# Kernel optimization log

Hardware: AMD Instinct MI355X
Metric: run time of the kernel (lower is better)

## Reference

```python
import jax, jax.numpy as jnp
import numpy as np

B, HW, ENC, E, D, A, V, L = 64, 14, 2048, 512, 512, 512, 32000, 32
LN_EPS = 1e-5


def setup_inputs() -> dict:
    key = jax.random.key(0)
    ks = jax.random.split(key, 16)
    s = 0.02
    n = lambda k, sh: jax.random.normal(k, sh, jnp.float32)
    encoder_out = n(ks[0], (B, HW, HW, ENC))
    encoded_captions = jax.random.randint(ks[1], (B, L), 0, V)
    caption_lengths = jax.random.randint(ks[2], (B, 1), 2, L + 1)
    caption_lengths = caption_lengths.at[0, 0].set(L)  # ensure max length present
    return dict(
        encoder_out=encoder_out,
        encoded_captions=encoded_captions,
        caption_lengths=caption_lengths,
        emb=n(ks[3], (V, E)) * s,
        W_enc_att=n(ks[4], (A, ENC)) * s, b_enc_att=jnp.zeros((A,)),
        W_dec_att=n(ks[5], (A, D)) * s, b_dec_att=jnp.zeros((A,)),
        W_full_att=n(ks[6], (1, A)) * s, b_full_att=jnp.zeros((1,)),
        W_ih=n(ks[7], (4 * D, E + ENC)) * s, b_ih=jnp.zeros((4 * D,)),
        W_hh=n(ks[8], (4 * D, D)) * s, b_hh=jnp.zeros((4 * D,)),
        g_h=jnp.ones((D,)), be_h=jnp.zeros((D,)),
        g_c=jnp.ones((D,)), be_c=jnp.zeros((D,)),
        W_init_h=n(ks[9], (D, ENC)) * s, b_init_h=jnp.zeros((D,)),
        W_init_c=n(ks[10], (D, ENC)) * s, b_init_c=jnp.zeros((D,)),
        W_beta=n(ks[11], (ENC, D)) * s, b_beta=jnp.zeros((ENC,)),
        W_fc=n(ks[12], (V, D)) * s, b_fc=jnp.zeros((V,)),
    )


def _layer_norm(x, g, b):
    m = x.mean(-1, keepdims=True)
    v = ((x - m) ** 2).mean(-1, keepdims=True)
    return (x - m) / jnp.sqrt(v + LN_EPS) * g + b


def reference(encoder_out, encoded_captions, caption_lengths, emb,
              W_enc_att, b_enc_att, W_dec_att, b_dec_att, W_full_att, b_full_att,
              W_ih, b_ih, W_hh, b_hh, g_h, be_h, g_c, be_c,
              W_init_h, b_init_h, W_init_c, b_init_c, W_beta, b_beta, W_fc, b_fc):
    bsz = encoder_out.shape[0]
    enc_out = encoder_out.reshape(bsz, -1, encoder_out.shape[-1])  # [B,P,ENC]
    lengths = caption_lengths[:, 0]
    order = jnp.argsort(-lengths)  # stable descending sort (matches torch sort)
    lengths = lengths[order]
    enc_out = enc_out[order]
    caps = encoded_captions[order]
    embeds = emb[caps]  # [B,L,E]
    decode_lengths = lengths - 1
    T = caps.shape[1] - 1  # static max(decode_lengths)

    mean_enc = enc_out.mean(axis=1)
    h = _layer_norm(mean_enc @ W_init_h.T + b_init_h, g_h, be_h)
    c = _layer_norm(mean_enc @ W_init_c.T + b_init_c, g_c, be_c)

    att1 = enc_out @ W_enc_att.T + b_enc_att  # [B,P,A] precomputed once
    prev_seq = jnp.swapaxes(embeds[:, :T], 0, 1)  # [T,B,E] teacher-forced inputs
    masks = jnp.arange(T)[:, None] < decode_lengths[None, :]  # [T,B] active rows

    def step(carry, xs):
        h, c = carry
        prev, mask = xs
        # attention
        att2 = h @ W_dec_att.T + b_dec_att  # [B,A]
        e = jax.nn.relu(att1 + att2[:, None, :]) @ W_full_att[0] + b_full_att[0]  # [B,P]
        alpha = jax.nn.softmax(e, axis=1)
        awe = jnp.einsum('bpe,bp->be', enc_out, alpha)  # [B,ENC]
        gate = jax.nn.sigmoid(h @ W_beta.T + b_beta)
        awe = gate * awe
        # LSTM cell
        x = jnp.concatenate([prev, awe], axis=1)  # [B,E+ENC]
        gates = x @ W_ih.T + b_ih + h @ W_hh.T + b_hh
        i, f, g, o = jnp.split(gates, 4, axis=1)
        c_new = jax.nn.sigmoid(f) * c + jax.nn.sigmoid(i) * jnp.tanh(g)
        h_new = jax.nn.sigmoid(o) * jnp.tanh(c_new)
        h_new = _layer_norm(h_new, g_h, be_h)
        c_new = _layer_norm(c_new, g_c, be_c)
        preds = h_new @ W_fc.T + b_fc  # [B,V]; dropout is identity in eval
        m = mask[:, None]
        h = jnp.where(m, h_new, h)  # freeze finished rows (== torch batch shrink)
        c = jnp.where(m, c_new, c)
        return (h, c), (jnp.where(m, preds, 0.0), jnp.where(m, alpha, 0.0))

    (_, _), (preds_t, alphas_t) = jax.lax.scan(step, (h, c), (prev_seq, masks))
    predictions = jnp.swapaxes(preds_t, 0, 1)  # [B,T,V]
    alphas = jnp.swapaxes(alphas_t, 0, 1)      # [B,T,P]
    return predictions, caps, decode_lengths, alphas, order
```

## Files before the change

kernel.cpp:

```cpp
#include <hip/hip_runtime.h>
#include <cfloat>
#include <math.h>

#define B_ 64
#define P_ 196
#define ENC_ 2048
#define D_ 512
#define V_ 32000
#define L_ 32
#define T_ 31

#define OUT_PREDS 0L
#define OUT_CAPS  63488000L
#define OUT_DECL  63490048L
#define OUT_ALPH  63490112L
#define OUT_ORDER 63878976L

typedef __bf16 bf16;
typedef __bf16 bf16x8 __attribute__((ext_vector_type(8)));
typedef __bf16 bf16x4 __attribute__((ext_vector_type(4)));
typedef float  f32x4  __attribute__((ext_vector_type(4)));

static __device__ __forceinline__ float sigmoidf_(float x) { return 1.f / (1.f + __expf(-x)); }

__global__ void k_order(const int* __restrict__ cap_len, const int* __restrict__ caps,
                        int* __restrict__ order_i, int* __restrict__ declen_i,
                        int* __restrict__ caps_i, float* __restrict__ out)
{
    __shared__ int len_s[B_];
    int tid = threadIdx.x;
    len_s[tid] = cap_len[tid];
    __syncthreads();
    int li = len_s[tid];
    int pos = 0;
    for (int j = 0; j < B_; ++j) {
        int lj = len_s[j];
        pos += (lj > li) || (lj == li && j < tid);
    }
    order_i[pos]  = tid;
    declen_i[pos] = li - 1;
    out[OUT_ORDER + pos] = (float)tid;
    out[OUT_DECL  + pos] = (float)(li - 1);
    for (int l = 0; l < L_; ++l) {
        int tok = caps[tid * L_ + l];
        caps_i[pos * L_ + l] = tok;
        out[OUT_CAPS + pos * L_ + l] = (float)tok;
    }
}

__global__ __launch_bounds__(256) void k_cvt(const float* __restrict__ in, bf16* __restrict__ ob, long n)
{
    long i = ((long)blockIdx.x * 256 + threadIdx.x) * 8;
    if (i >= n) return;
    float4 a = *(const float4*)(in + i);
    float4 b = *(const float4*)(in + i + 4);
    bf16x8 v;
    v[0]=(bf16)a.x; v[1]=(bf16)a.y; v[2]=(bf16)a.z; v[3]=(bf16)a.w;
    v[4]=(bf16)b.x; v[5]=(bf16)b.y; v[6]=(bf16)b.z; v[7]=(bf16)b.w;
    *(bf16x8*)(ob + i) = v;
}

__global__ __launch_bounds__(256) void k_cvt_enc(const float* __restrict__ enc,
                                                 const int* __restrict__ order_i,
                                                 bf16* __restrict__ enc_s)
{
    long i = ((long)blockIdx.x * 256 + threadIdx.x) * 8;
    int b = (int)(i / ((long)P_ * ENC_));
    long rem = i - (long)b * P_ * ENC_;
    const float* src = enc + (long)order_i[b] * P_ * ENC_ + rem;
    float4 a = *(const float4*)(src);
    float4 c = *(const float4*)(src + 4);
    bf16x8 v;
    v[0]=(bf16)a.x; v[1]=(bf16)a.y; v[2]=(bf16)a.z; v[3]=(bf16)a.w;
    v[4]=(bf16)c.x; v[5]=(bf16)c.y; v[6]=(bf16)c.z; v[7]=(bf16)c.w;
    *(bf16x8*)(enc_s + i) = v;
}

__global__ __launch_bounds__(256) void k_meanb(const bf16* __restrict__ enc_s, bf16* __restrict__ mean_b)
{
    int b = blockIdx.x, col = blockIdx.y * 256 + threadIdx.x;
    float s = 0.f;
    const bf16* eb = enc_s + (long)b * P_ * ENC_ + col;
    for (int p = 0; p < P_; ++p) s += (float)eb[(long)p * ENC_];
    mean_b[(long)b * ENC_ + col] = (bf16)(s * (1.f / (float)P_));
}

template<int FUSE, int EPI, int SWZ>
__global__ void __launch_bounds__(256)
k_mgemm(const bf16* __restrict__ A, long lda,
        const bf16* __restrict__ B1, const bf16* __restrict__ B2,
        const float* __restrict__ bias,
        float* __restrict__ Cf, bf16* __restrict__ Cb,
        int N, int K, int kspl, int Nsp, int Ksp,
        const int* __restrict__ declen_i)
{
    const int tid = threadIdx.x;
    const int lane = tid & 63, w = tid >> 6;
    int mt, nt, z;
    if (SWZ == 0)      { mt = blockIdx.x; nt = blockIdx.y; z = blockIdx.z; }
    else if (SWZ == 1) { int o = blockIdx.x; int wg = (o & 7) * 98 + (o >> 3);
                         mt = wg >> 2; nt = wg & 3; z = 0; }
    else               { int o = blockIdx.x; int xcd = o & 7;
                         int base = xcd < 6 ? xcd * 969 : 5814 + (xcd - 6) * 968;
                         int wg = base + (o >> 3);
                         nt = wg / 31; mt = wg - 31 * nt; z = 0; }
    const int krange = K / kspl;
    const int k0 = z * krange, k1 = k0 + krange;
    const int r16 = lane & 15, kq = lane >> 4;
    const int koff = kq * 8;

    const bf16* Ap = A + (long)(mt * 64 + r16) * lda + koff;
    const int ncol0 = nt * 128 + w * 32;

    const bf16* Bp[2];
    const bf16* B2p[2];
#pragma unroll
    for (int ni = 0; ni < 2; ++ni) {
        int n = ncol0 + ni * 16 + r16;
        if (FUSE == 1)
            Bp[ni] = (n < Nsp) ? B1 + (long)n * K + koff
                               : B2 + (long)(n - Nsp) * K + koff;
        else if (FUSE == 2) {
            Bp[ni]  = B1 + (long)n * Ksp + koff;
            B2p[ni] = B2 + (long)n * (K - Ksp) + koff - Ksp;
        } else
            Bp[ni] = B1 + (long)n * K + koff;
    }

    auto loadA = [&](int kk, bf16x8* dst) {
#pragma unroll
        for (int mi = 0; mi < 4; ++mi)
            dst[mi] = *(const bf16x8*)(Ap + (long)mi * 16 * lda + kk);
    };
    auto loadB = [&](int kk, bf16x8* dst) {
#pragma unroll
        for (int ni = 0; ni < 2; ++ni) {
            if (FUSE == 2 && kk >= Ksp) dst[ni] = *(const bf16x8*)(B2p[ni] + kk);
            else                        dst[ni] = *(const bf16x8*)(Bp[ni] + kk);
        }
    };

    f32x4 acc[4][2] = {};
    bf16x8 af[4], bfr[2];
    loadA(k0, af); loadB(k0, bfr);
    for (int kk = k0 + 32; kk < k1; kk += 32) {
        bf16x8 af2[4], bf2[2];
        loadA(kk, af2); loadB(kk, bf2);
#pragma unroll
        for (int mi = 0; mi < 4; ++mi)
#pragma unroll
            for (int ni = 0; ni < 2; ++ni)
                acc[mi][ni] = __builtin_amdgcn_mfma_f32_16x16x32_bf16(af[mi], bfr[ni], acc[mi][ni], 0, 0, 0);
#pragma unroll
        for (int mi = 0; mi < 4; ++mi) af[mi] = af2[mi];
#pragma unroll
        for (int ni = 0; ni < 2; ++ni) bfr[ni] = bf2[ni];
    }
#pragma unroll
    for (int mi = 0; mi < 4; ++mi)
#pragma unroll
        for (int ni = 0; ni < 2; ++ni)
            acc[mi][ni] = __builtin_amdgcn_mfma_f32_16x16x32_bf16(af[mi], bfr[ni], acc[mi][ni], 0, 0, 0);

#pragma unroll
    for (int mi = 0; mi < 4; ++mi) {
#pragma unroll
        for (int ni = 0; ni < 2; ++ni) {
            int col = ncol0 + ni * 16 + r16;
#pragma unroll
            for (int r = 0; r < 4; ++r) {
                int row = mt * 64 + mi * 16 + kq * 4 + r;
                float v = acc[mi][ni][r];
                if (EPI == 0) {
                    Cf[(long)z * 64 * N + (long)row * N + col] = v;
                } else if (EPI == 1) {
                    Cb[(long)row * N + col] = (bf16)(v + bias[col]);
                } else {
                    int tt = row >> 6, b = row & 63;
                    bool msk = tt < declen_i[b];
                    Cf[OUT_PREDS + ((long)b * T_ + tt) * V_ + col] = msk ? (v + bias[col]) : 0.f;
                }
            }
        }
    }
}

static __device__ __forceinline__ void ln_stats(float x, float* r1, float* r2,
                                                float& m, float& var)
{
    int tid = threadIdx.x;
    r1[tid] = x; r2[tid] = x * x;
    __syncthreads();
    for (int s = 256; s > 0; s >>= 1) {
        if (tid < s) { r1[tid] += r1[tid + s]; r2[tid] += r2[tid + s]; }
        __syncthreads();
    }
    m = r1[0] * (1.f / 512.f);
    var = r2[0] * (1.f / 512.f) - m * m;
    __syncthreads();
}

__global__ __launch_bounds__(512)
void k_initln(const float* __restrict__ pi,
              const float* __restrict__ b_h, const float* __restrict__ b_c,
              const float* __restrict__ g_h, const float* __restrict__ be_h,
              const float* __restrict__ g_c, const float* __restrict__ be_c,
              bf16* __restrict__ xh, float* __restrict__ c)
{
    int b = blockIdx.x, d = threadIdx.x;
    float yh = pi[(long)b * 1024 + d]       + b_h[d];
    float yc = pi[(long)b * 1024 + 512 + d] + b_c[d];
    __shared__ float r1[512], r2[512];
    float m, v;
    ln_stats(yh, r1, r2, m, v);
    xh[(long)b * 3072 + 2560 + d] = (bf16)((yh - m) * rsqrtf(v + 1e-5f) * g_h[d] + be_h[d]);
    ln_stats(yc, r1, r2, m, v);
    c[(long)b * 512 + d] = (yc - m) * rsqrtf(v + 1e-5f) * g_c[d] + be_c[d];
}

__global__ __launch_bounds__(512)
void k_attn(const float* __restrict__ att2gate, const float* __restrict__ b_dec,
            const float* __restrict__ b_beta, const float* __restrict__ Wfull,
            const bf16* __restrict__ att1_b, const bf16* __restrict__ enc_s,
            const int* __restrict__ caps_i, const int* __restrict__ declen_i,
            const float* __restrict__ emb,
            bf16* __restrict__ xh, float* __restrict__ out, int t)
{
    const int b = blockIdx.x, tid = threadIdx.x;
    __shared__ float att2s[512], wf[512], red[512];
    __shared__ float alp[P_];
    {
        float s = b_dec[tid];
#pragma unroll
        for (int zz = 0; zz < 4; ++zz) s += att2gate[((long)zz * 64 + b) * 2560 + tid];
        att2s[tid] = s;
        wf[tid] = Wfull[tid];
    }
    __syncthreads();
    float ev = -FLT_MAX;
    if (tid < P_) {
        const bf16* ar = att1_b + ((long)b * P_ + tid) * 512;
        float acc = 0.f;
        for (int a0 = 0; a0 < 512; a0 += 8) {
            bf16x8 v = *(const bf16x8*)(ar + a0);
#pragma unroll
            for (int j = 0; j < 8; ++j)
                acc += fmaxf((float)v[j] + att2s[a0 + j], 0.f) * wf[a0 + j];
        }
        ev = acc;
    }
    red[tid] = ev;
    __syncthreads();
    for (int s = 256; s > 0; s >>= 1) { if (tid < s) red[tid] = fmaxf(red[tid], red[tid + s]); __syncthreads(); }
    float mx = red[0];
    __syncthreads();
    float ex = (tid < P_) ? __expf(ev - mx) : 0.f;
    red[tid] = ex;
    __syncthreads();
    for (int s = 256; s > 0; s >>= 1) { if (tid < s) red[tid] += red[tid + s]; __syncthreads(); }
    float inv = 1.f / red[0];
    bool msk = t < declen_i[b];
    if (tid < P_) {
        float al = ex * inv;
        alp[tid] = al;
        out[OUT_ALPH + ((long)b * T_ + t) * P_ + tid] = msk ? al : 0.f;
    }
    __syncthreads();
    const int col = tid * 4;
    float a0 = 0.f, a1 = 0.f, a2 = 0.f, a3 = 0.f;
    const bf16* eb = enc_s + (long)b * P_ * ENC_ + col;
#pragma unroll 4
    for (int p = 0; p < P_; ++p) {
        bf16x4 v = *(const bf16x4*)(eb + (long)p * ENC_);
        float al = alp[p];
        a0 += al * (float)v[0]; a1 += al * (float)v[1];
        a2 += al * (float)v[2]; a3 += al * (float)v[3];
    }
    float av[4] = {a0, a1, a2, a3};
#pragma unroll
    for (int j = 0; j < 4; ++j) {
        float gpre = b_beta[col + j];
#pragma unroll
        for (int zz = 0; zz < 4; ++zz) gpre += att2gate[((long)zz * 64 + b) * 2560 + 512 + col + j];
        xh[(long)b * 3072 + 512 + col + j] = (bf16)(av[j] * sigmoidf_(gpre));
    }
    int tok = caps_i[b * L_ + t];
    xh[(long)b * 3072 + tid] = (bf16)emb[(long)tok * 512 + tid];
}

__global__ __launch_bounds__(512)
void k_lstm(const float* __restrict__ gp, const float* __restrict__ b_ih, const float* __restrict__ b_hh,
            const float* __restrict__ g_h, const float* __restrict__ be_h,
            const float* __restrict__ g_c, const float* __restrict__ be_c,
            bf16* __restrict__ xh, float* __restrict__ c, bf16* __restrict__ hseq,
            const int* __restrict__ declen_i, int t)
{
    int b = blockIdx.x, d = threadIdx.x;
    float iv = b_ih[d]        + b_hh[d];
    float fv = b_ih[512 + d]  + b_hh[512 + d];
    float gv = b_ih[1024 + d] + b_hh[1024 + d];
    float ov = b_ih[1536 + d] + b_hh[1536 + d];
    for (int s = 0; s < 8; ++s) {
        const float* gs = gp + ((long)s * B_ + b) * 2048;
        iv += gs[d]; fv += gs[512 + d]; gv += gs[1024 + d]; ov += gs[1536 + d];
    }
    float cn = sigmoidf_(fv) * c[(long)b * 512 + d] + sigmoidf_(iv) * tanhf(gv);
    float hn = sigmoidf_(ov) * tanhf(cn);
    __shared__ float r1[512], r2[512];
    float m, v;
    ln_stats(hn, r1, r2, m, v);
    float hln = (hn - m) * rsqrtf(v + 1e-5f) * g_h[d] + be_h[d];
    ln_stats(cn, r1, r2, m, v);
    float cln = (cn - m) * rsqrtf(v + 1e-5f) * g_c[d] + be_c[d];
    bool msk = t < declen_i[b];
    bf16 hold = xh[(long)b * 3072 + 2560 + d];
    bf16 hv = msk ? (bf16)hln : hold;
    xh[(long)b * 3072 + 2560 + d] = hv;
    hseq[((long)t * B_ + b) * 512 + d] = hv;
    if (msk) c[(long)b * 512 + d] = cln;
}

extern "C" void kernel_launch(void* const* d_in, const int* in_sizes, int n_in,
                              void* d_out, int out_size, void* d_ws, size_t ws_size,
                              hipStream_t stream)
{
    const float* enc       = (const float*)d_in[0];
    const int*   caps      = (const int*)  d_in[1];
    const int*   caplen    = (const int*)  d_in[2];
    const float* emb       = (const float*)d_in[3];
    const float* W_enc_att = (const float*)d_in[4];
    const float* b_enc_att = (const float*)d_in[5];
    const float* W_dec_att = (const float*)d_in[6];
    const float* b_dec_att = (const float*)d_in[7];
    const float* W_full    = (const float*)d_in[8];
    const float* W_ih      = (const float*)d_in[10];
    const float* b_ih      = (const float*)d_in[11];
    const float* W_hh      = (const float*)d_in[12];
    const float* b_hh      = (const float*)d_in[13];
    const float* g_h       = (const float*)d_in[14];
    const float* be_h      = (const float*)d_in[15];
    const float* g_c       = (const float*)d_in[16];
    const float* be_c      = (const float*)d_in[17];
    const float* W_init_h  = (const float*)d_in[18];
    const float* b_init_h  = (const float*)d_in[19];
    const float* W_init_c  = (const float*)d_in[20];
    const float* b_init_c  = (const float*)d_in[21];
    const float* W_beta    = (const float*)d_in[22];
    const float* b_beta    = (const float*)d_in[23];
    const float* W_fc      = (const float*)d_in[24];
    const float* b_fc      = (const float*)d_in[25];
    float* out = (float*)d_out;

    char* w = (char*)d_ws;
    auto alloc = [&](size_t bytes) { char* p = w; w += (bytes + 255) & ~(size_t)255; return p; };
    int*   order_i  = (int*)  alloc(B_ * 4);
    int*   declen_i = (int*)  alloc(B_ * 4);
    int*   caps_i   = (int*)  alloc(B_ * L_ * 4);
    bf16*  enc_s    = (bf16*) alloc((size_t)B_ * P_ * ENC_ * 2);
    bf16*  mean_b   = (bf16*) alloc((size_t)B_ * ENC_ * 2);
    bf16*  att1_b   = (bf16*) alloc((size_t)B_ * P_ * 512 * 2);
    float* pi       = (float*)alloc((size_t)B_ * 1024 * 4);
    float* att2gate = (float*)alloc((size_t)4 * B_ * 2560 * 4);
    bf16*  xh       = (bf16*) alloc((size_t)B_ * 3072 * 2);
    float* gp       = (float*)alloc((size_t)8 * B_ * 2048 * 4);
    float* cbuf     = (float*)alloc((size_t)B_ * 512 * 4);
    bf16*  hseq     = (bf16*) alloc((size_t)T_ * B_ * 512 * 2);
    bf16*  W_enc_b  = (bf16*) alloc((size_t)512 * 2048 * 2);
    bf16*  W_dec_b  = (bf16*) alloc((size_t)512 * 512 * 2);
    bf16*  W_beta_b = (bf16*) alloc((size_t)2048 * 512 * 2);
    bf16*  W_ih_b   = (bf16*) alloc((size_t)2048 * 2560 * 2);
    bf16*  W_hh_b   = (bf16*) alloc((size_t)2048 * 512 * 2);
    bf16*  W_fc_b   = (bf16*) alloc((size_t)32000 * 512 * 2);
    bf16*  W_inh_b  = (bf16*) alloc((size_t)512 * 2048 * 2);
    bf16*  W_inc_b  = (bf16*) alloc((size_t)512 * 2048 * 2);

    k_order<<<1, B_, 0, stream>>>(caplen, caps, order_i, declen_i, caps_i, out);
    k_cvt_enc<<<12544, 256, 0, stream>>>(enc, order_i, enc_s);
    k_meanb<<<dim3(B_, 8), 256, 0, stream>>>(enc_s, mean_b);

    auto cvt = [&](const float* src, bf16* dst, long n) {
        k_cvt<<<(int)((n / 8 + 255) / 256), 256, 0, stream>>>(src, dst, n);
    };
    cvt(W_enc_att, W_enc_b, 512L * 2048);
    cvt(W_dec_att, W_dec_b, 512L * 512);
    cvt(W_beta,    W_beta_b, 2048L * 512);
    cvt(W_ih,      W_ih_b,  2048L * 2560);
    cvt(W_hh,      W_hh_b,  2048L * 512);
    cvt(W_fc,      W_fc_b,  32000L * 512);
    cvt(W_init_h,  W_inh_b, 512L * 2048);
    cvt(W_init_c,  W_inc_b, 512L * 2048);

    k_mgemm<1, 0, 0><<<dim3(1, 8, 1), 256, 0, stream>>>(mean_b, 2048, W_inh_b, W_inc_b,
        nullptr, pi, nullptr, 1024, 2048, 1, 512, 0, nullptr);
    k_initln<<<B_, 512, 0, stream>>>(pi, b_init_h, b_init_c, g_h, be_h, g_c, be_c, xh, cbuf);

    k_mgemm<0, 1, 1><<<784, 256, 0, stream>>>(enc_s, 2048, W_enc_b, nullptr,
        b_enc_att, nullptr, att1_b, 512, 2048, 1, 0, 0, nullptr);

    for (int t = 0; t < T_; ++t) {
        k_mgemm<1, 0, 0><<<dim3(1, 20, 4), 256, 0, stream>>>(xh + 2560, 3072, W_dec_b, W_beta_b,
            nullptr, att2gate, nullptr, 2560, 512, 4, 512, 0, nullptr);
        k_attn<<<B_, 512, 0, stream>>>(att2gate, b_dec_att, b_beta, W_full, att1_b, enc_s,
            caps_i, declen_i, emb, xh, out, t);
        k_mgemm<2, 0, 0><<<dim3(1, 16, 8), 256, 0, stream>>>(xh, 3072, W_ih_b, W_hh_b,
            nullptr, gp, nullptr, 2048, 3072, 8, 0, 2560, nullptr);
        k_lstm<<<B_, 512, 0, stream>>>(gp, b_ih, b_hh, g_h, be_h, g_c, be_c,
            xh, cbuf, hseq, declen_i, t);
    }

    k_mgemm<0, 2, 2><<<7750, 256, 0, stream>>>(hseq, 512, W_fc_b, nullptr,
        b_fc, out, nullptr, V_, 512, 1, 0, 0, declen_i);
}
```

Baseline: 2.493 ms.

## Split attention into alpha and weighted-sum kernels, skip finished rows, vectorize GEMM epilogue

The per-step attention kernel is split in two: k_alpha computes the scores and softmax with 256 threads, and k_awe computes the alpha-weighted encoder sum across a 4x wider grid, which gives the memory-bound reduction over enc_s more blocks. Rows whose caption has already finished now exit early in the attention and LSTM kernels, which skips their work and their enc_s reads. The MFMA operands are swapped so each lane holds four consecutive columns, allowing vectorized f32x4/bf16x4 stores in the GEMM epilogues. In exchange this adds one kernel launch per step and an alpha buffer round trip through global memory, and it relies on finished rows being left untouched in the buffers.

Measured after the change: 2.516 ms. No clear change (+0.9%).

```diff
diff --git a/kernel.cpp b/kernel.cpp
--- a/kernel.cpp
+++ b/kernel.cpp
@@ -19,6 +19,7 @@
 typedef __bf16 bf16;
 typedef __bf16 bf16x8 __attribute__((ext_vector_type(8)));
 typedef __bf16 bf16x4 __attribute__((ext_vector_type(4)));
+typedef __bf16 bf16x2 __attribute__((ext_vector_type(2)));
 typedef float  f32x4  __attribute__((ext_vector_type(4)));
 
 static __device__ __forceinline__ float sigmoidf_(float x) { return 1.f / (1.f + __expf(-x)); }
@@ -150,7 +151,7 @@
         for (int mi = 0; mi < 4; ++mi)
 #pragma unroll
             for (int ni = 0; ni < 2; ++ni)
-                acc[mi][ni] = __builtin_amdgcn_mfma_f32_16x16x32_bf16(af[mi], bfr[ni], acc[mi][ni], 0, 0, 0);
+                acc[mi][ni] = __builtin_amdgcn_mfma_f32_16x16x32_bf16(bfr[ni], af[mi], acc[mi][ni], 0, 0, 0);
 #pragma unroll
         for (int mi = 0; mi < 4; ++mi) af[mi] = af2[mi];
 #pragma unroll
@@ -160,26 +161,31 @@
     for (int mi = 0; mi < 4; ++mi)
 #pragma unroll
         for (int ni = 0; ni < 2; ++ni)
-            acc[mi][ni] = __builtin_amdgcn_mfma_f32_16x16x32_bf16(af[mi], bfr[ni], acc[mi][ni], 0, 0, 0);
+            acc[mi][ni] = __builtin_amdgcn_mfma_f32_16x16x32_bf16(bfr[ni], af[mi], acc[mi][ni], 0, 0, 0);
 
 #pragma unroll
     for (int mi = 0; mi < 4; ++mi) {
+        const int row = mt * 64 + mi * 16 + r16;
 #pragma unroll
         for (int ni = 0; ni < 2; ++ni) {
-            int col = ncol0 + ni * 16 + r16;
-#pragma unroll
-            for (int r = 0; r < 4; ++r) {
-                int row = mt * 64 + mi * 16 + kq * 4 + r;
-                float v = acc[mi][ni][r];
-                if (EPI == 0) {
-                    Cf[(long)z * 64 * N + (long)row * N + col] = v;
-                } else if (EPI == 1) {
-                    Cb[(long)row * N + col] = (bf16)(v + bias[col]);
-                } else {
-                    int tt = row >> 6, b = row & 63;
-                    bool msk = tt < declen_i[b];
-                    Cf[OUT_PREDS + ((long)b * T_ + tt) * V_ + col] = msk ? (v + bias[col]) : 0.f;
-                }
+            const int col = ncol0 + ni * 16 + kq * 4;
+            f32x4 v = acc[mi][ni];
+            if (EPI == 0) {
+                *(f32x4*)(Cf + (long)z * 64 * N + (long)row * N + col) = v;
+            } else if (EPI == 1) {
+                f32x4 bv = *(const f32x4*)(bias + col);
+                bf16x4 o;
+                o[0]=(bf16)(v[0]+bv[0]); o[1]=(bf16)(v[1]+bv[1]);
+                o[2]=(bf16)(v[2]+bv[2]); o[3]=(bf16)(v[3]+bv[3]);
+                *(bf16x4*)(Cb + (long)row * N + col) = o;
+            } else {
+                int tt = row >> 6, b = row & 63;
+                bool msk = tt < declen_i[b];
+                f32x4 bv = *(const f32x4*)(bias + col);
+                f32x4 o;
+                o[0] = msk ? v[0]+bv[0] : 0.f; o[1] = msk ? v[1]+bv[1] : 0.f;
+                o[2] = msk ? v[2]+bv[2] : 0.f; o[3] = msk ? v[3]+bv[3] : 0.f;
+                *(f32x4*)(Cf + OUT_PREDS + ((long)b * T_ + tt) * V_ + col) = o;
             }
         }
     }
@@ -218,23 +224,25 @@
     c[(long)b * 512 + d] = (yc - m) * rsqrtf(v + 1e-5f) * g_c[d] + be_c[d];
 }
 
-__global__ __launch_bounds__(512)
-void k_attn(const float* __restrict__ att2gate, const float* __restrict__ b_dec,
-            const float* __restrict__ b_beta, const float* __restrict__ Wfull,
-            const bf16* __restrict__ att1_b, const bf16* __restrict__ enc_s,
-            const int* __restrict__ caps_i, const int* __restrict__ declen_i,
-            const float* __restrict__ emb,
-            bf16* __restrict__ xh, float* __restrict__ out, int t)
+__global__ __launch_bounds__(256)
+void k_alpha(const float* __restrict__ att2gate, const float* __restrict__ b_dec,
+             const float* __restrict__ Wfull, const bf16* __restrict__ att1_b,
+             const int* __restrict__ caps_i, const int* __restrict__ declen_i,
+             const float* __restrict__ emb, float* __restrict__ alpha_b,
+             bf16* __restrict__ xh, float* __restrict__ out, int t)
 {
     const int b = blockIdx.x, tid = threadIdx.x;
-    __shared__ float att2s[512], wf[512], red[512];
-    __shared__ float alp[P_];
-    {
-        float s = b_dec[tid];
-#pragma unroll
-        for (int zz = 0; zz < 4; ++zz) s += att2gate[((long)zz * 64 + b) * 2560 + tid];
-        att2s[tid] = s;
-        wf[tid] = Wfull[tid];
+    if (t >= declen_i[b]) {
+        if (tid < P_) out[OUT_ALPH + ((long)b * T_ + t) * P_ + tid] = 0.f;
+        return;
+    }
+    __shared__ float att2s[512], wf[512], red[256];
+    for (int i = tid; i < 512; i += 256) {
+        float s = b_dec[i];
+#pragma unroll
+        for (int zz = 0; zz < 4; ++zz) s += att2gate[((long)zz * 64 + b) * 2560 + i];
+        att2s[i] = s;
+        wf[i] = Wfull[i];
     }
     __syncthreads();
     float ev = -FLT_MAX;
@@ -251,41 +259,53 @@
     }
     red[tid] = ev;
     __syncthreads();
-    for (int s = 256; s > 0; s >>= 1) { if (tid < s) red[tid] = fmaxf(red[tid], red[tid + s]); __syncthreads(); }
+    for (int s = 128; s > 0; s >>= 1) { if (tid < s) red[tid] = fmaxf(red[tid], red[tid + s]); __syncthreads(); }
     float mx = red[0];
     __syncthreads();
     float ex = (tid < P_) ? __expf(ev - mx) : 0.f;
     red[tid] = ex;
     __syncthreads();
-    for (int s = 256; s > 0; s >>= 1) { if (tid < s) red[tid] += red[tid + s]; __syncthreads(); }
+    for (int s = 128; s > 0; s >>= 1) { if (tid < s) red[tid] += red[tid + s]; __syncthreads(); }
     float inv = 1.f / red[0];
-    bool msk = t < declen_i[b];
     if (tid < P_) {
         float al = ex * inv;
-        alp[tid] = al;
-        out[OUT_ALPH + ((long)b * T_ + t) * P_ + tid] = msk ? al : 0.f;
-    }
-    __syncthreads();
-    const int col = tid * 4;
-    float a0 = 0.f, a1 = 0.f, a2 = 0.f, a3 = 0.f;
+        alpha_b[b * P_ + tid] = al;
+        out[OUT_ALPH + ((long)b * T_ + t) * P_ + tid] = al;
+    }
+    int tok = caps_i[b * L_ + t];
+    for (int i = tid; i < 512; i += 256)
+        xh[(long)b * 3072 + i] = (bf16)emb[(long)tok * 512 + i];
+}
+
+__global__ __launch_bounds__(256)
+void k_awe(const float* __restrict__ alpha_b, const float* __restrict__ att2gate,
+           const float* __restrict__ b_beta, const bf16* __restrict__ enc_s,
+           const int* __restrict__ declen_i, bf16* __restrict__ xh, int t)
+{
+    const int b = blockIdx.x, tid = threadIdx.x;
+    if (t >= declen_i[b]) return;
+    __shared__ float alp[P_];
+    if (tid < P_) alp[tid] = alpha_b[b * P_ + tid];
+    __syncthreads();
+    const int col = blockIdx.y * 512 + tid * 2;
     const bf16* eb = enc_s + (long)b * P_ * ENC_ + col;
+    float a0 = 0.f, a1 = 0.f;
 #pragma unroll 4
     for (int p = 0; p < P_; ++p) {
-        bf16x4 v = *(const bf16x4*)(eb + (long)p * ENC_);
+        bf16x2 v = *(const bf16x2*)(eb + (long)p * ENC_);
         float al = alp[p];
         a0 += al * (float)v[0]; a1 += al * (float)v[1];
-        a2 += al * (float)v[2]; a3 += al * (float)v[3];
-    }
-    float av[4] = {a0, a1, a2, a3};
-#pragma unroll
-    for (int j = 0; j < 4; ++j) {
-        float gpre = b_beta[col + j];
-#pragma unroll
-        for (int zz = 0; zz < 4; ++zz) gpre += att2gate[((long)zz * 64 + b) * 2560 + 512 + col + j];
-        xh[(long)b * 3072 + 512 + col + j] = (bf16)(av[j] * sigmoidf_(gpre));
-    }
-    int tok = caps_i[b * L_ + t];
-    xh[(long)b * 3072 + tid] = (bf16)emb[(long)tok * 512 + tid];
+    }
+    float g0 = b_beta[col], g1 = b_beta[col + 1];
+#pragma unroll
+    for (int zz = 0; zz < 4; ++zz) {
+        const float* gs = att2gate + ((long)zz * 64 + b) * 2560 + 512 + col;
+        g0 += gs[0]; g1 += gs[1];
+    }
+    bf16x2 o;
+    o[0] = (bf16)(a0 * sigmoidf_(g0));
+    o[1] = (bf16)(a1 * sigmoidf_(g1));
+    *(bf16x2*)(xh + (long)b * 3072 + 512 + col) = o;
 }
 
 __global__ __launch_bounds__(512)
@@ -296,6 +316,7 @@
             const int* __restrict__ declen_i, int t)
 {
     int b = blockIdx.x, d = threadIdx.x;
+    if (t >= declen_i[b]) return;
     float iv = b_ih[d]        + b_hh[d];
     float fv = b_ih[512 + d]  + b_hh[512 + d];
     float gv = b_ih[1024 + d] + b_hh[1024 + d];
@@ -312,12 +333,10 @@
     float hln = (hn - m) * rsqrtf(v + 1e-5f) * g_h[d] + be_h[d];
     ln_stats(cn, r1, r2, m, v);
     float cln = (cn - m) * rsqrtf(v + 1e-5f) * g_c[d] + be_c[d];
-    bool msk = t < declen_i[b];
-    bf16 hold = xh[(long)b * 3072 + 2560 + d];
-    bf16 hv = msk ? (bf16)hln : hold;
+    bf16 hv = (bf16)hln;
     xh[(long)b * 3072 + 2560 + d] = hv;
     hseq[((long)t * B_ + b) * 512 + d] = hv;
-    if (msk) c[(long)b * 512 + d] = cln;
+    c[(long)b * 512 + d] = cln;
 }
 
 extern "C" void kernel_launch(void* const* d_in, const int* in_sizes, int n_in,
@@ -361,6 +380,7 @@
     bf16*  att1_b   = (bf16*) alloc((size_t)B_ * P_ * 512 * 2);
     float* pi       = (float*)alloc((size_t)B_ * 1024 * 4);
     float* att2gate = (float*)alloc((size_t)4 * B_ * 2560 * 4);
+    float* alpha_b  = (float*)alloc((size_t)B_ * P_ * 4);
     bf16*  xh       = (bf16*) alloc((size_t)B_ * 3072 * 2);
     float* gp       = (float*)alloc((size_t)8 * B_ * 2048 * 4);
     float* cbuf     = (float*)alloc((size_t)B_ * 512 * 4);
@@ -400,8 +420,10 @@
     for (int t = 0; t < T_; ++t) {
         k_mgemm<1, 0, 0><<<dim3(1, 20, 4), 256, 0, stream>>>(xh + 2560, 3072, W_dec_b, W_beta_b,
             nullptr, att2gate, nullptr, 2560, 512, 4, 512, 0, nullptr);
-        k_attn<<<B_, 512, 0, stream>>>(att2gate, b_dec_att, b_beta, W_full, att1_b, enc_s,
-            caps_i, declen_i, emb, xh, out, t);
+        k_alpha<<<B_, 256, 0, stream>>>(att2gate, b_dec_att, W_full, att1_b,
+            caps_i, declen_i, emb, alpha_b, xh, out, t);
+        k_awe<<<dim3(B_, 4), 256, 0, stream>>>(alpha_b, att2gate, b_beta, enc_s,
+            declen_i, xh, t);
         k_mgemm<2, 0, 0><<<dim3(1, 16, 8), 256, 0, stream>>>(xh, 3072, W_ih_b, W_hh_b,
             nullptr, gp, nullptr, 2048, 3072, 8, 0, 2560, nullptr);
         k_lstm<<<B_, 512, 0, stream>>>(gp, b_ih, b_hh, g_h, be_h, g_c, be_c,
```
